# Optimization experiments

Hardware: AMD Instinct MI355X
Metric: run time of the kernel (lower is better)

The kernel has to match this reference:

```python
import jax, jax.numpy as jnp
import numpy as np

D_MODEL = 1024
NUM_HEADS = 16
HEAD_DIM = D_MODEL // NUM_HEADS


def setup_inputs() -> dict:
    key = jax.random.key(0)
    ks = jax.random.split(key, 10)
    B, S, D = 2, 2048, D_MODEL
    s = 1.0 / np.sqrt(D)
    return {
        "x": jax.random.normal(ks[0], (B, S, D), dtype=jnp.float32),
        "q_w": jax.random.normal(ks[1], (D, D), dtype=jnp.float32) * s,
        "q_b": jnp.zeros((D,), dtype=jnp.float32),
        "k_w": jax.random.normal(ks[2], (D, D), dtype=jnp.float32) * s,
        "k_b": jnp.zeros((D,), dtype=jnp.float32),
        "v_w": jax.random.normal(ks[3], (D, D), dtype=jnp.float32) * s,
        "v_b": jnp.zeros((D,), dtype=jnp.float32),
        "out_w": jax.random.normal(ks[4], (D, D), dtype=jnp.float32) * s,
        "out_b": jnp.zeros((D,), dtype=jnp.float32),
        "evidence_scale": jnp.ones((1,), dtype=jnp.float32),
        "evidence_bias": jnp.zeros((1,), dtype=jnp.float32),
    }


def reference(x, q_w, q_b, k_w, k_b, v_w, v_b, out_w, out_b, evidence_scale, evidence_bias):
    B, S, D = x.shape
    H, Hd = NUM_HEADS, HEAD_DIM

    def proj(w, b):  # torch Linear: x @ w.T + b, then split heads -> [B,H,S,Hd]
        y = jnp.einsum('bsd,ed->bse', x, w) + b
        return y.reshape(B, S, H, Hd).transpose(0, 2, 1, 3)

    Q = proj(q_w, q_b)
    K = proj(k_w, k_b)
    V = proj(v_w, v_b)

    scores = jnp.einsum('bhqd,bhkd->bhqk', Q, K) / np.sqrt(Hd)  # [B,H,S,S]
    evidence = jnp.exp(scores) * evidence_scale + 1.0 + evidence_bias
    denom = evidence.sum(axis=-1, keepdims=True)                # [B,H,S,1]
    uncertainty = S / denom                                     # [B,H,S,1]
    probs = evidence / denom

    attn = jnp.einsum('bhqk,bhkd->bhqd', probs, V)              # [B,H,S,Hd]
    attn = attn.transpose(0, 2, 1, 3).reshape(B, S, D)
    output = jnp.einsum('bsd,ed->bse', attn, out_w) + out_b
    return output, jnp.squeeze(uncertainty, -1)
```

## Files before the change

### kernel.cpp

```cpp
#include <hip/hip_runtime.h>

typedef __attribute__((ext_vector_type(8))) short bf16x8;
typedef __attribute__((ext_vector_type(4))) float f32x4;

constexpr int Dm  = 1024;
constexpr int NH  = 16;
constexpr int HD  = 64;
constexpr int SQ  = 2048;
constexpr int BB  = 2;
constexpr int MM  = BB * SQ;

__device__ __forceinline__ unsigned short f2bf(float f) {
    unsigned int u = __float_as_uint(f);
    u += 0x7FFFu + ((u >> 16) & 1u);
    return (unsigned short)(u >> 16);
}

__device__ __forceinline__ void gld16(const void* g, void* l) {
    __builtin_amdgcn_global_load_lds(
        (const __attribute__((address_space(1))) void*)g,
        (__attribute__((address_space(3))) void*)l, 16, 0, 0);
}

__global__ void cast_all(const float4* __restrict__ x,  const float4* __restrict__ qw,
                         const float4* __restrict__ kw, const float4* __restrict__ vw,
                         const float4* __restrict__ ow,
                         uint2* __restrict__ xb,  uint2* __restrict__ qwb,
                         uint2* __restrict__ kwb, uint2* __restrict__ vwb,
                         uint2* __restrict__ owb)
{
    int i = blockIdx.x * 256 + threadIdx.x;
    const float4* src; uint2* dst; int off;
    if      (i < 1048576) { src = x;  dst = xb;  off = i; }
    else if (i < 1310720) { src = qw; dst = qwb; off = i - 1048576; }
    else if (i < 1572864) { src = kw; dst = kwb; off = i - 1310720; }
    else if (i < 1835008) { src = vw; dst = vwb; off = i - 1572864; }
    else                  { src = ow; dst = owb; off = i - 1835008; }
    float4 v = src[off];
    uint2 o;
    o.x = (unsigned)f2bf(v.x) | ((unsigned)f2bf(v.y) << 16);
    o.y = (unsigned)f2bf(v.z) | ((unsigned)f2bf(v.w) << 16);
    dst[off] = o;
}

template<typename EPI>
__device__ __forceinline__ void gemm_core(const unsigned short* __restrict__ A,
                                          const unsigned short* __restrict__ W,
                                          const float* __restrict__ bias,
                                          int n0, int m0, EPI epi)
{
    __shared__ unsigned short As[128 * 32];
    __shared__ unsigned short Ws[128 * 32];
    const int t    = threadIdx.x;
    const int lane = t & 63, w = t >> 6;
    const int lm   = lane & 15, quad = lane >> 4;
    const int wm   = w & 1, wn = w >> 1;

    const f32x4 fz = {0.f, 0.f, 0.f, 0.f};
    f32x4 acc[4][4];
#pragma unroll
    for (int mi = 0; mi < 4; ++mi)
#pragma unroll
        for (int ni = 0; ni < 4; ++ni) acc[mi][ni] = fz;

    float bsv[4];
#pragma unroll
    for (int ni = 0; ni < 4; ++ni) bsv[ni] = bias[n0 + wn * 64 + ni * 16 + lm];

    const int r0 = t >> 2,         ks0 = t & 3;
    const int r1 = (t + 256) >> 2, ks1 = (t + 256) & 3;

    for (int k0 = 0; k0 < 1024; k0 += 32) {
        __syncthreads();
        gld16(A + (size_t)(m0 + r0) * 1024 + k0 + ks0 * 8, &As[t * 8]);
        gld16(A + (size_t)(m0 + r1) * 1024 + k0 + ks1 * 8, &As[(t + 256) * 8]);
        gld16(W + (size_t)(n0 + r0) * 1024 + k0 + ks0 * 8, &Ws[t * 8]);
        gld16(W + (size_t)(n0 + r1) * 1024 + k0 + ks1 * 8, &Ws[(t + 256) * 8]);
        __syncthreads();

        bf16x8 af[4], bfr[4];
#pragma unroll
        for (int mi = 0; mi < 4; ++mi)
            af[mi] = *(const bf16x8*)&As[(wm * 64 + mi * 16 + lm) * 32 + quad * 8];
#pragma unroll
        for (int ni = 0; ni < 4; ++ni)
            bfr[ni] = *(const bf16x8*)&Ws[(wn * 64 + ni * 16 + lm) * 32 + quad * 8];
#pragma unroll
        for (int mi = 0; mi < 4; ++mi)
#pragma unroll
            for (int ni = 0; ni < 4; ++ni)
                acc[mi][ni] = __builtin_amdgcn_mfma_f32_16x16x32_bf16(
                                  af[mi], bfr[ni], acc[mi][ni], 0, 0, 0);
    }

#pragma unroll
    for (int mi = 0; mi < 4; ++mi)
#pragma unroll
        for (int ni = 0; ni < 4; ++ni)
#pragma unroll
            for (int r = 0; r < 4; ++r) {
                const int m = m0 + wm * 64 + mi * 16 + quad * 4 + r;
                const int n = n0 + wn * 64 + ni * 16 + lm;
                epi(m, n, acc[mi][ni][r] + bsv[ni]);
            }
}

__global__ __launch_bounds__(256) void gemm_qkv(
    const unsigned short* __restrict__ xb,
    const unsigned short* __restrict__ qwb, const float* __restrict__ qb,
    const unsigned short* __restrict__ kwb, const float* __restrict__ kb,
    const unsigned short* __restrict__ vwb, const float* __restrict__ vb,
    unsigned short* __restrict__ Qb, unsigned short* __restrict__ Kb,
    unsigned short* __restrict__ Vb)
{
    const int z = blockIdx.z;
    const unsigned short* W = (z == 0) ? qwb : (z == 1) ? kwb : vwb;
    const float* bias       = (z == 0) ? qb  : (z == 1) ? kb  : vb;
    unsigned short* dst     = (z == 0) ? Qb  : (z == 1) ? Kb  : Vb;
    const int n0 = blockIdx.x * 128, m0 = blockIdx.y * 128;
    const bool vt = (z == 2);

    gemm_core(xb, W, bias, n0, m0, [&](int m, int n, float v) {
        const int b = m >> 11, s = m & 2047, h = n >> 6, hd = n & 63;
        const size_t idx = vt ? ((size_t)((b * NH + h) * 64 + hd) * SQ + s)
                              : ((size_t)((b * NH + h) * SQ + s) * 64 + hd);
        dst[idx] = f2bf(v);
    });
}

__global__ __launch_bounds__(256) void gemm_out(
    const unsigned short* __restrict__ Ab, const unsigned short* __restrict__ owb,
    const float* __restrict__ ob, float* __restrict__ out)
{
    const int n0 = blockIdx.x * 128, m0 = blockIdx.y * 128;
    gemm_core(Ab, owb, ob, n0, m0, [&](int m, int n, float v) {
        out[(size_t)m * 1024 + n] = v;
    });
}

constexpr int ST = 88;

__global__ __launch_bounds__(256) void attn_mfma(const unsigned short* __restrict__ Qg,
                                                 const unsigned short* __restrict__ Kg,
                                                 const unsigned short* __restrict__ Vtg,
                                                 const float* __restrict__ esc,
                                                 const float* __restrict__ ebi,
                                                 unsigned short* __restrict__ Ab,
                                                 float* __restrict__ unc)
{
    __shared__ unsigned short Qs[64 * ST];
    __shared__ unsigned short Ks[64 * ST];
    __shared__ unsigned short Vts[64 * ST];
    __shared__ unsigned short Es[4 * 16 * ST];
    __shared__ float dred[64][17];
    __shared__ float dinv[64];

    const int t    = threadIdx.x;
    const int lane = t & 63, w = t >> 6;
    const int lm   = lane & 15, quad = lane >> 4;
    const int qt   = blockIdx.x & 31;
    const int bh   = blockIdx.x >> 5;
    const int q0   = qt * 64;

    const float scale = esc[0];
    const float bias1 = 1.0f + ebi[0];

    {
        const unsigned short* g = Qg + (size_t)(bh * SQ + q0) * 64;
#pragma unroll
        for (int i = 0; i < 2; ++i) {
            int seg = t + 256 * i, r = seg >> 3, c8 = seg & 7;
            *(uint4*)&Qs[r * ST + c8 * 8] = *(const uint4*)(g + r * 64 + c8 * 8);
        }
    }

    const f32x4 fz = {0.f, 0.f, 0.f, 0.f};
    f32x4 acc[4];
#pragma unroll
    for (int ni = 0; ni < 4; ++ni) acc[ni] = fz;
    float drow[4] = {0.f, 0.f, 0.f, 0.f};

    for (int kt = 0; kt < 32; ++kt) {
        __syncthreads();
        {
            const unsigned short* kg = Kg  + (size_t)(bh * SQ + kt * 64) * 64;
            const unsigned short* vg = Vtg + (size_t)bh * 64 * SQ + kt * 64;
#pragma unroll
            for (int i = 0; i < 2; ++i) {
                int seg = t + 256 * i, r = seg >> 3, c8 = seg & 7;
                *(uint4*)&Ks[r * ST + c8 * 8]  = *(const uint4*)(kg + r * 64 + c8 * 8);
                *(uint4*)&Vts[r * ST + c8 * 8] = *(const uint4*)(vg + (size_t)r * SQ + c8 * 8);
            }
        }
        __syncthreads();

        bf16x8 qa[2];
#pragma unroll
        for (int kc = 0; kc < 2; ++kc)
            qa[kc] = *(const bf16x8*)&Qs[(w * 16 + lm) * ST + kc * 32 + quad * 8];
#pragma unroll
        for (int ni = 0; ni < 4; ++ni) {
            f32x4 s = fz;
#pragma unroll
            for (int kc = 0; kc < 2; ++kc) {
                bf16x8 kb = *(const bf16x8*)&Ks[(ni * 16 + lm) * ST + kc * 32 + quad * 8];
                s = __builtin_amdgcn_mfma_f32_16x16x32_bf16(qa[kc], kb, s, 0, 0, 0);
            }
#pragma unroll
            for (int r = 0; r < 4; ++r) {
                float ev = __expf(s[r] * 0.125f) * scale + bias1;
                drow[r] += ev;
                Es[w * 16 * ST + (quad * 4 + r) * ST + ni * 16 + lm] = f2bf(ev);
            }
        }
        __syncthreads();

        bf16x8 ea[2];
#pragma unroll
        for (int kc = 0; kc < 2; ++kc)
            ea[kc] = *(const bf16x8*)&Es[w * 16 * ST + lm * ST + kc * 32 + quad * 8];
#pragma unroll
        for (int ni = 0; ni < 4; ++ni)
#pragma unroll
            for (int kc = 0; kc < 2; ++kc) {
                bf16x8 vb = *(const bf16x8*)&Vts[(ni * 16 + lm) * ST + kc * 32 + quad * 8];
                acc[ni] = __builtin_amdgcn_mfma_f32_16x16x32_bf16(ea[kc], vb, acc[ni], 0, 0, 0);
            }
    }

    __syncthreads();
#pragma unroll
    for (int r = 0; r < 4; ++r)
        dred[w * 16 + quad * 4 + r][lm] = drow[r];
    __syncthreads();
    if (t < 64) {
        float d = 0.f;
#pragma unroll
        for (int c = 0; c < 16; ++c) d += dred[t][c];
        unc[(size_t)bh * SQ + q0 + t] = (float)SQ / d;
        dinv[t] = 1.0f / d;
    }
    __syncthreads();

    const int b = bh >> 4, h = bh & 15;
#pragma unroll
    for (int ni = 0; ni < 4; ++ni)
#pragma unroll
        for (int r = 0; r < 4; ++r) {
            const int q = w * 16 + quad * 4 + r;
            const float v = acc[ni][r] * dinv[q];
            Ab[(size_t)(b * SQ + q0 + q) * Dm + h * 64 + ni * 16 + lm] = f2bf(v);
        }
}

extern "C" void kernel_launch(void* const* d_in, const int* in_sizes, int n_in,
                              void* d_out, int out_size, void* d_ws, size_t ws_size,
                              hipStream_t stream)
{
    const float* x   = (const float*)d_in[0];
    const float* qw  = (const float*)d_in[1];
    const float* qb  = (const float*)d_in[2];
    const float* kw  = (const float*)d_in[3];
    const float* kb  = (const float*)d_in[4];
    const float* vw  = (const float*)d_in[5];
    const float* vb  = (const float*)d_in[6];
    const float* ow  = (const float*)d_in[7];
    const float* ob  = (const float*)d_in[8];
    const float* esc = (const float*)d_in[9];
    const float* ebi = (const float*)d_in[10];

    float* out = (float*)d_out;
    float* unc = out + (size_t)MM * Dm;

    unsigned short* xb  = (unsigned short*)d_ws;
    unsigned short* qwb = (unsigned short*)((char*)d_ws + (8u  << 20));
    unsigned short* kwb = (unsigned short*)((char*)d_ws + (10u << 20));
    unsigned short* vwb = (unsigned short*)((char*)d_ws + (12u << 20));
    unsigned short* owb = (unsigned short*)((char*)d_ws + (14u << 20));
    unsigned short* Vb  = (unsigned short*)((char*)d_ws + (16u << 20));
    unsigned short* Ab  = xb;

    unsigned short* Qb = (unsigned short*)d_out;
    unsigned short* Kb = Qb + (size_t)MM * Dm;

    cast_all<<<dim3(2097152 / 256), dim3(256), 0, stream>>>(
        (const float4*)x, (const float4*)qw, (const float4*)kw,
        (const float4*)vw, (const float4*)ow,
        (uint2*)xb, (uint2*)qwb, (uint2*)kwb, (uint2*)vwb, (uint2*)owb);

    gemm_qkv<<<dim3(Dm / 128, MM / 128, 3), dim3(256), 0, stream>>>(
        xb, qwb, qb, kwb, kb, vwb, vb, Qb, Kb, Vb);

    attn_mfma<<<dim3(BB * NH * (SQ / 64)), dim3(256), 0, stream>>>(
        Qb, Kb, Vb, esc, ebi, Ab, unc);

    gemm_out<<<dim3(Dm / 128, MM / 128), dim3(256), 0, stream>>>(Ab, owb, ob, out);
}
```

Before: 249.8 us.

## Split attention warps over query and key halves with direct LDS loads

Restructures the attention kernel so each wave handles 32 queries against half of each 64-key tile. Q is held in registers straight from global memory, and K/V^T tiles are loaded with global_load_lds into fragment-ordered LDS, which removes the padded staging and the Q shared buffer. Each wave writes its own exp tile to LDS and reads it back without a block barrier, leaving two barriers per tile instead of three. Partial outputs and denominators from the two key-halves are reduced through reused shared memory at the end, at the cost of an extra LDS reduction and some idle waves in the epilogue.

```diff
diff --git a/kernel.cpp b/kernel.cpp
--- a/kernel.cpp
+++ b/kernel.cpp
@@ -138,7 +138,7 @@
     });
 }
 
-constexpr int ST = 88;
+constexpr int STE = 40;
 
 __global__ __launch_bounds__(256) void attn_mfma(const unsigned short* __restrict__ Qg,
                                                  const unsigned short* __restrict__ Kg,
@@ -148,16 +148,18 @@
                                                  unsigned short* __restrict__ Ab,
                                                  float* __restrict__ unc)
 {
-    __shared__ unsigned short Qs[64 * ST];
-    __shared__ unsigned short Ks[64 * ST];
-    __shared__ unsigned short Vts[64 * ST];
-    __shared__ unsigned short Es[4 * 16 * ST];
-    __shared__ float dred[64][17];
+    __shared__ __align__(16) unsigned short sm[4096 + 4096 + 4 * 32 * STE];
     __shared__ float dinv[64];
+    unsigned short* Ks  = sm;
+    unsigned short* Vts = sm + 4096;
+    unsigned short* Es  = sm + 8192;
+    float* Ored  = (float*)sm;
+    float* dredA = (float*)(sm + 8192);
 
     const int t    = threadIdx.x;
     const int lane = t & 63, w = t >> 6;
     const int lm   = lane & 15, quad = lane >> 4;
+    const int wq   = w & 1, wk = w >> 1;
     const int qt   = blockIdx.x & 31;
     const int bh   = blockIdx.x >> 5;
     const int q0   = qt * 64;
@@ -165,92 +167,119 @@
     const float scale = esc[0];
     const float bias1 = 1.0f + ebi[0];
 
-    {
-        const unsigned short* g = Qg + (size_t)(bh * SQ + q0) * 64;
-#pragma unroll
-        for (int i = 0; i < 2; ++i) {
-            int seg = t + 256 * i, r = seg >> 3, c8 = seg & 7;
-            *(uint4*)&Qs[r * ST + c8 * 8] = *(const uint4*)(g + r * 64 + c8 * 8);
-        }
-    }
+    bf16x8 qa[2][2];
+#pragma unroll
+    for (int mi = 0; mi < 2; ++mi)
+#pragma unroll
+        for (int kc = 0; kc < 2; ++kc)
+            qa[mi][kc] = *(const bf16x8*)(Qg +
+                (size_t)(bh * SQ + q0 + wq * 32 + mi * 16 + lm) * 64 + kc * 32 + quad * 8);
 
     const f32x4 fz = {0.f, 0.f, 0.f, 0.f};
-    f32x4 acc[4];
-#pragma unroll
-    for (int ni = 0; ni < 4; ++ni) acc[ni] = fz;
-    float drow[4] = {0.f, 0.f, 0.f, 0.f};
+    f32x4 acc[2][4];
+#pragma unroll
+    for (int mi = 0; mi < 2; ++mi)
+#pragma unroll
+        for (int nd = 0; nd < 4; ++nd) acc[mi][nd] = fz;
+    float drow[2][4] = {};
+
+    const unsigned short* EsW = Es + w * 32 * STE;
 
     for (int kt = 0; kt < 32; ++kt) {
         __syncthreads();
         {
-            const unsigned short* kg = Kg  + (size_t)(bh * SQ + kt * 64) * 64;
-            const unsigned short* vg = Vtg + (size_t)bh * 64 * SQ + kt * 64;
-#pragma unroll
-            for (int i = 0; i < 2; ++i) {
-                int seg = t + 256 * i, r = seg >> 3, c8 = seg & 7;
-                *(uint4*)&Ks[r * ST + c8 * 8]  = *(const uint4*)(kg + r * 64 + c8 * 8);
-                *(uint4*)&Vts[r * ST + c8 * 8] = *(const uint4*)(vg + (size_t)r * SQ + c8 * 8);
-            }
+            const unsigned short* kg = Kg + (size_t)(bh * SQ + kt * 64) * 64
+                                     + (size_t)(w * 16 + lm) * 64 + quad * 8;
+            gld16(kg,      &Ks[(w * 2 + 0) * 512]);
+            gld16(kg + 32, &Ks[(w * 2 + 1) * 512]);
+            const unsigned short* vg = Vtg + (size_t)bh * 64 * SQ + kt * 64
+                                     + (size_t)(w * 16 + lm) * SQ + quad * 8;
+            gld16(vg,      &Vts[(w * 2 + 0) * 512]);
+            gld16(vg + 32, &Vts[(w * 2 + 1) * 512]);
         }
         __syncthreads();
 
-        bf16x8 qa[2];
-#pragma unroll
-        for (int kc = 0; kc < 2; ++kc)
-            qa[kc] = *(const bf16x8*)&Qs[(w * 16 + lm) * ST + kc * 32 + quad * 8];
-#pragma unroll
-        for (int ni = 0; ni < 4; ++ni) {
-            f32x4 s = fz;
-#pragma unroll
-            for (int kc = 0; kc < 2; ++kc) {
-                bf16x8 kb = *(const bf16x8*)&Ks[(ni * 16 + lm) * ST + kc * 32 + quad * 8];
-                s = __builtin_amdgcn_mfma_f32_16x16x32_bf16(qa[kc], kb, s, 0, 0, 0);
+        bf16x8 kbf[2][2];
+#pragma unroll
+        for (int ni = 0; ni < 2; ++ni)
+#pragma unroll
+            for (int kc = 0; kc < 2; ++kc)
+                kbf[ni][kc] = *(const bf16x8*)&Ks[((wk * 2 + ni) * 2 + kc) * 512 + lane * 8];
+
+#pragma unroll
+        for (int mi = 0; mi < 2; ++mi)
+#pragma unroll
+            for (int ni = 0; ni < 2; ++ni) {
+                f32x4 s = fz;
+#pragma unroll
+                for (int kc = 0; kc < 2; ++kc)
+                    s = __builtin_amdgcn_mfma_f32_16x16x32_bf16(qa[mi][kc], kbf[ni][kc], s, 0, 0, 0);
+#pragma unroll
+                for (int r = 0; r < 4; ++r) {
+                    float ev = __expf(s[r] * 0.125f) * scale + bias1;
+                    drow[mi][r] += ev;
+                    ((unsigned short*)EsW)[(mi * 16 + quad * 4 + r) * STE + ni * 16 + lm] = f2bf(ev);
+                }
             }
-#pragma unroll
-            for (int r = 0; r < 4; ++r) {
-                float ev = __expf(s[r] * 0.125f) * scale + bias1;
-                drow[r] += ev;
-                Es[w * 16 * ST + (quad * 4 + r) * ST + ni * 16 + lm] = f2bf(ev);
-            }
+
+        bf16x8 ea[2];
+#pragma unroll
+        for (int mi = 0; mi < 2; ++mi)
+            ea[mi] = *(const bf16x8*)&EsW[(mi * 16 + lm) * STE + quad * 8];
+#pragma unroll
+        for (int nd = 0; nd < 4; ++nd) {
+            bf16x8 vbf = *(const bf16x8*)&Vts[(nd * 2 + wk) * 512 + lane * 8];
+#pragma unroll
+            for (int mi = 0; mi < 2; ++mi)
+                acc[mi][nd] = __builtin_amdgcn_mfma_f32_16x16x32_bf16(ea[mi], vbf, acc[mi][nd], 0, 0, 0);
         }
-        __syncthreads();
-
-        bf16x8 ea[2];
-#pragma unroll
-        for (int kc = 0; kc < 2; ++kc)
-            ea[kc] = *(const bf16x8*)&Es[w * 16 * ST + lm * ST + kc * 32 + quad * 8];
-#pragma unroll
-        for (int ni = 0; ni < 4; ++ni)
-#pragma unroll
-            for (int kc = 0; kc < 2; ++kc) {
-                bf16x8 vb = *(const bf16x8*)&Vts[(ni * 16 + lm) * ST + kc * 32 + quad * 8];
-                acc[ni] = __builtin_amdgcn_mfma_f32_16x16x32_bf16(ea[kc], vb, acc[ni], 0, 0, 0);
-            }
     }
 
     __syncthreads();
-#pragma unroll
-    for (int r = 0; r < 4; ++r)
-        dred[w * 16 + quad * 4 + r][lm] = drow[r];
+    if (wk == 1) {
+#pragma unroll
+        for (int mi = 0; mi < 2; ++mi)
+#pragma unroll
+            for (int nd = 0; nd < 4; ++nd)
+#pragma unroll
+                for (int r = 0; r < 4; ++r)
+                    Ored[wq * 2048 + (mi * 16 + quad * 4 + r) * 64 + nd * 16 + lm] = acc[mi][nd][r];
+    }
+#pragma unroll
+    for (int mi = 0; mi < 2; ++mi)
+#pragma unroll
+        for (int r = 0; r < 4; ++r)
+            dredA[w * 512 + (mi * 16 + quad * 4 + r) * 16 + lm] = drow[mi][r];
     __syncthreads();
+
     if (t < 64) {
+        const int wq2 = t >> 5, ql = t & 31;
         float d = 0.f;
 #pragma unroll
-        for (int c = 0; c < 16; ++c) d += dred[t][c];
+        for (int k2 = 0; k2 < 2; ++k2)
+#pragma unroll
+            for (int c = 0; c < 16; ++c)
+                d += dredA[(k2 * 2 + wq2) * 512 + ql * 16 + c];
         unc[(size_t)bh * SQ + q0 + t] = (float)SQ / d;
         dinv[t] = 1.0f / d;
     }
     __syncthreads();
 
-    const int b = bh >> 4, h = bh & 15;
-#pragma unroll
-    for (int ni = 0; ni < 4; ++ni)
-#pragma unroll
-        for (int r = 0; r < 4; ++r) {
-            const int q = w * 16 + quad * 4 + r;
-            const float v = acc[ni][r] * dinv[q];
-            Ab[(size_t)(b * SQ + q0 + q) * Dm + h * 64 + ni * 16 + lm] = f2bf(v);
-        }
+    if (wk == 0) {
+        const int b = bh >> 4, h = bh & 15;
+#pragma unroll
+        for (int mi = 0; mi < 2; ++mi)
+#pragma unroll
+            for (int nd = 0; nd < 4; ++nd)
+#pragma unroll
+                for (int r = 0; r < 4; ++r) {
+                    const int ql = mi * 16 + quad * 4 + r;
+                    const int q  = wq * 32 + ql;
+                    const float v = (acc[mi][nd][r] + Ored[wq * 2048 + ql * 64 + nd * 16 + lm])
+                                    * dinv[q];
+                    Ab[(size_t)(b * SQ + q0 + q) * Dm + h * 64 + nd * 16 + lm] = f2bf(v);
+                }
+    }
 }
 
 extern "C" void kernel_launch(void* const* d_in, const int* in_sizes, int n_in,
```

New measurement: 259.0 us. 1.04x slower.
